# Kernel tuning notes

Measured on AMD Instinct MI355X. Metric: run time of the kernel, lower is better.

Reference implementation:

```python
import jax, jax.numpy as jnp
import numpy as np

EMBED_SIZE = 768
HEAD_SIZE = 64
B, T = 4, 2048


def setup_inputs() -> dict:
    key = jax.random.key(0)
    kx, kk, kq, kv = jax.random.split(key, 4)
    x = jax.random.normal(kx, (B, T, EMBED_SIZE), dtype=jnp.float32)
    # torch Linear(E, H, bias=False): weight [H, E]; stored here as [E, H] for x @ W
    s = 1.0 / np.sqrt(EMBED_SIZE)
    Wk = jax.random.uniform(kk, (EMBED_SIZE, HEAD_SIZE), jnp.float32, -s, s)
    Wq = jax.random.uniform(kq, (EMBED_SIZE, HEAD_SIZE), jnp.float32, -s, s)
    Wv = jax.random.uniform(kv, (EMBED_SIZE, HEAD_SIZE), jnp.float32, -s, s)
    return {"x": x, "Wk": Wk, "Wq": Wq, "Wv": Wv}


def reference(x, Wk, Wq, Wv):
    Bx, Tx, E = x.shape
    k = x @ Wk  # [B, T, H]
    q = x @ Wq
    v = x @ Wv
    w = jnp.einsum("bth,bsh->bts", q, k)  # [B, T, T]
    causal = jnp.tril(jnp.ones((Tx, Tx), dtype=bool))
    # Faithful to source: mask to -inf FIRST, then scale by sqrt(embed_size)
    w = jnp.where(causal, w, -jnp.inf)
    w = w / jnp.sqrt(jnp.asarray(E, dtype=x.dtype))
    w = jax.nn.softmax(w, axis=-1)
    # dropout: eval mode / identity for the correctness baseline
    return jnp.einsum("bts,bsh->bth", w, v)
```

## Files before the change

kernel.cpp:

```cpp
#include <hip/hip_runtime.h>
#include <hip/hip_bf16.h>


typedef __attribute__((ext_vector_type(8))) short short8;
typedef __attribute__((ext_vector_type(4))) float f32x4;

#define SPLIT_KB 8
#define MAX_SP 5

__device__ __forceinline__ unsigned short f2bf(float f) {
    union { float f; unsigned u; } v; v.f = f;
    unsigned r = v.u + 0x7fffu + ((v.u >> 16) & 1u);
    return (unsigned short)(r >> 16);
}

__global__ __launch_bounds__(256) void wt_kernel(const float* __restrict__ Wk,
                                                 const float* __restrict__ Wq,
                                                 const float* __restrict__ Wv,
                                                 unsigned short* __restrict__ WT) {
    const float CSCALE = 1.4426950408889634f / 27.712812921102035f;
    int flat = blockIdx.x * 256 + threadIdx.x;
    int k = flat / 192, n = flat % 192;
    int mat = n >> 6, col = n & 63;
    const float* W = (mat == 0) ? Wq : (mat == 1) ? Wk : Wv;
    float v = W[k * 64 + col];
    if (mat == 0) v *= CSCALE;
    WT[n * 768 + k] = f2bf(v);
}

__global__ __launch_bounds__(256) void proj_kernel(const float* __restrict__ x,
                                                   const unsigned short* __restrict__ WT,
                                                   unsigned short* __restrict__ qws,
                                                   unsigned short* __restrict__ kws,
                                                   unsigned short* __restrict__ vT) {
    __shared__ unsigned short xs[64 * 72];
    __shared__ unsigned short wsm[64 * 72];
    int tid = threadIdx.x;
    int lane = tid & 63, wave = tid >> 6;
    int quad = lane >> 4, l16 = lane & 15;
    int wm = wave & 1, wn = wave >> 1;
    int row0 = blockIdx.x * 64;
    int my = blockIdx.y;

    f32x4 acc[2][2];
    for (int mt = 0; mt < 2; ++mt)
        for (int nt = 0; nt < 2; ++nt) acc[mt][nt] = (f32x4)(0.f);

    for (int kc = 0; kc < 12; ++kc) {
        __syncthreads();
        for (int i = 0; i < 2; ++i) {
            int e = tid + 256 * i;
            int row = e >> 3, hb = (e & 7) * 8;
            const float* src = x + (size_t)(row0 + row) * 768 + kc * 64 + hb;
            float4 f0 = *(const float4*)(src);
            float4 f1 = *(const float4*)(src + 4);
            short8 pk;
            pk[0] = (short)f2bf(f0.x); pk[1] = (short)f2bf(f0.y);
            pk[2] = (short)f2bf(f0.z); pk[3] = (short)f2bf(f0.w);
            pk[4] = (short)f2bf(f1.x); pk[5] = (short)f2bf(f1.y);
            pk[6] = (short)f2bf(f1.z); pk[7] = (short)f2bf(f1.w);
            *(short8*)&xs[row * 72 + hb] = pk;
        }
        for (int i = 0; i < 2; ++i) {
            int e = tid + 256 * i;
            int n = e >> 3, kb8 = (e & 7) * 8;
            *(short8*)&wsm[n * 72 + kb8] =
                *(const short8*)&WT[(size_t)(my * 64 + n) * 768 + kc * 64 + kb8];
        }
        __syncthreads();
        for (int kh = 0; kh < 2; ++kh) {
            int kk = kh * 32 + quad * 8;
            short8 a[2], bfr[2];
            for (int mt = 0; mt < 2; ++mt)
                a[mt] = *(const short8*)&xs[(wm * 32 + mt * 16 + l16) * 72 + kk];
            for (int nt = 0; nt < 2; ++nt)
                bfr[nt] = *(const short8*)&wsm[(wn * 32 + nt * 16 + l16) * 72 + kk];
            for (int mt = 0; mt < 2; ++mt)
                for (int nt = 0; nt < 2; ++nt)
                    acc[mt][nt] = __builtin_amdgcn_mfma_f32_16x16x32_bf16(
                        a[mt], bfr[nt], acc[mt][nt], 0, 0, 0);
        }
    }
    __syncthreads();
    for (int mt = 0; mt < 2; ++mt) {
        for (int nt = 0; nt < 2; ++nt) {
            int n = wn * 32 + nt * 16 + l16;
            for (int j = 0; j < 4; ++j) {
                int rloc = wm * 32 + mt * 16 + quad * 4 + j;
                unsigned short bv = f2bf(acc[mt][nt][j]);
                if (my == 0)      qws[(size_t)(row0 + rloc) * 64 + n] = bv;
                else if (my == 1) kws[(size_t)(row0 + rloc) * 64 + n] = bv;
                else              xs[n * 72 + rloc] = bv;
            }
        }
    }
    if (my == 2) {
        __syncthreads();
        int bidx = row0 >> 11, t0 = row0 & 2047;
        for (int i = 0; i < 2; ++i) {
            int e = tid + 256 * i;
            int c = e >> 3, rb = (e & 7) * 8;
            *(short8*)&vT[((size_t)(bidx * 64 + c)) * 2048 + t0 + rb] =
                *(const short8*)&xs[c * 72 + rb];
        }
    }
}

__global__ __launch_bounds__(128) void attn_split(const unsigned short* __restrict__ qws,
                                                  const unsigned short* __restrict__ kws,
                                                  const unsigned short* __restrict__ vT,
                                                  float* __restrict__ po,
                                                  float* __restrict__ pm,
                                                  float* __restrict__ pl) {
    int bx = blockIdx.x, b = blockIdx.y, sp = blockIdx.z;
    int kbmax = (bx >> 1) + 1;
    int nsp = (kbmax + SPLIT_KB - 1) / SPLIT_KB;
    if (sp >= nsp) return;
    int kb_lo = sp * SPLIT_KB;
    int kb_hi = min(kb_lo + SPLIT_KB, kbmax);

    __shared__ unsigned short qs[32 * 72];
    __shared__ unsigned short ks[64 * 72];
    __shared__ unsigned short vs[64 * 72];
    __shared__ unsigned short ps[2][16 * 72];
    int tid = threadIdx.x;
    int lane = tid & 63, wave = tid >> 6;
    int quad = lane >> 4, l16 = lane & 15;
    int q0 = bx * 32;
    size_t qbase = ((size_t)b * 2048 + q0) * 64;
    for (int i = 0; i < 2; ++i) {
        int e = tid + 128 * i;
        int r = e >> 3, hb = (e & 7) * 8;
        *(short8*)&qs[r * 72 + hb] = *(const short8*)&qws[qbase + r * 64 + hb];
    }
    __syncthreads();
    short8 aq[2];
    for (int kh = 0; kh < 2; ++kh)
        aq[kh] = *(const short8*)&qs[(wave * 16 + l16) * 72 + kh * 32 + quad * 8];

    f32x4 o_acc[4];
    for (int nt = 0; nt < 4; ++nt) o_acc[nt] = (f32x4)(0.f);
    float m_run[4], l_run[4];
    int row_g[4];
    for (int j = 0; j < 4; ++j) {
        m_run[j] = -1e30f; l_run[j] = 0.f;
        row_g[j] = q0 + wave * 16 + quad * 4 + j;
    }

    for (int kb = kb_lo; kb < kb_hi; ++kb) {
        __syncthreads();
        size_t kvbase = ((size_t)b * 2048 + kb * 64) * 64;
        for (int i = 0; i < 4; ++i) {
            int e = tid + 128 * i;
            int r = e >> 3, hb = (e & 7) * 8;
            *(short8*)&ks[r * 72 + hb] = *(const short8*)&kws[kvbase + r * 64 + hb];
        }
        for (int i = 0; i < 4; ++i) {
            int e = tid + 128 * i;
            int h = e >> 3, kyb = (e & 7) * 8;
            *(short8*)&vs[h * 72 + kyb] =
                *(const short8*)&vT[((size_t)b * 64 + h) * 2048 + kb * 64 + kyb];
        }
        __syncthreads();
        f32x4 s[4];
        for (int nt = 0; nt < 4; ++nt) s[nt] = (f32x4)(0.f);
        for (int kh = 0; kh < 2; ++kh)
            for (int nt = 0; nt < 4; ++nt) {
                short8 bk = *(const short8*)&ks[(nt * 16 + l16) * 72 + kh * 32 + quad * 8];
                s[nt] = __builtin_amdgcn_mfma_f32_16x16x32_bf16(aq[kh], bk, s[nt], 0, 0, 0);
            }
        if (kb == kbmax - 1) {
            for (int nt = 0; nt < 4; ++nt) {
                int key = kb * 64 + nt * 16 + l16;
                for (int j = 0; j < 4; ++j)
                    if (key > row_g[j]) s[nt][j] = -1e30f;
            }
        }
        float mx[4], al[4], rs[4];
        for (int j = 0; j < 4; ++j)
            mx[j] = fmaxf(fmaxf(s[0][j], s[1][j]), fmaxf(s[2][j], s[3][j]));
        for (int off = 1; off < 16; off <<= 1)
            for (int j = 0; j < 4; ++j)
                mx[j] = fmaxf(mx[j], __shfl_xor(mx[j], off, 16));
        for (int j = 0; j < 4; ++j) {
            float mn = fmaxf(m_run[j], mx[j]);
            al[j] = exp2f(m_run[j] - mn);
            m_run[j] = mn;
            rs[j] = 0.f;
        }
        for (int nt = 0; nt < 4; ++nt)
            for (int j = 0; j < 4; ++j) {
                float p = exp2f(s[nt][j] - m_run[j]);
                rs[j] += p;
                ps[wave][(quad * 4 + j) * 72 + nt * 16 + l16] = f2bf(p);
            }
        for (int off = 1; off < 16; off <<= 1)
            for (int j = 0; j < 4; ++j)
                rs[j] += __shfl_xor(rs[j], off, 16);
        for (int j = 0; j < 4; ++j) l_run[j] = l_run[j] * al[j] + rs[j];
        for (int nt = 0; nt < 4; ++nt)
            for (int j = 0; j < 4; ++j) o_acc[nt][j] *= al[j];
        for (int kh = 0; kh < 2; ++kh) {
            short8 ap = *(const short8*)&ps[wave][l16 * 72 + kh * 32 + quad * 8];
            for (int nt = 0; nt < 4; ++nt) {
                short8 bv = *(const short8*)&vs[(nt * 16 + l16) * 72 + kh * 32 + quad * 8];
                o_acc[nt] = __builtin_amdgcn_mfma_f32_16x16x32_bf16(ap, bv, o_acc[nt], 0, 0, 0);
            }
        }
    }
    int sbase = ((b * 64 + bx) * MAX_SP + sp) * 32;
    for (int nt = 0; nt < 4; ++nt)
        for (int j = 0; j < 4; ++j) {
            int r = wave * 16 + quad * 4 + j;
            po[(size_t)(sbase + r) * 64 + nt * 16 + l16] = o_acc[nt][j];
        }
    if (l16 == 0) {
        for (int j = 0; j < 4; ++j) {
            int r = wave * 16 + quad * 4 + j;
            pm[sbase + r] = m_run[j];
            pl[sbase + r] = l_run[j];
        }
    }
}

__global__ __launch_bounds__(256) void reduce_kernel(const float* __restrict__ po,
                                                     const float* __restrict__ pm,
                                                     const float* __restrict__ pl,
                                                     float* __restrict__ out) {
    int tid = threadIdx.x;
    int lane = tid & 63, wave = tid >> 6;
    int g = blockIdx.x * 4 + wave;
    int b = g >> 11, t = g & 2047;
    int bx = t >> 5, r = t & 31;
    int kbmax = (bx >> 1) + 1;
    int nsp = (kbmax + SPLIT_KB - 1) / SPLIT_KB;
    int base = ((b * 64 + bx) * MAX_SP) * 32 + r;
    float mstar = -1e30f;
    for (int sp = 0; sp < nsp; ++sp)
        mstar = fmaxf(mstar, pm[base + sp * 32]);
    float acc = 0.f, lsum = 0.f;
    for (int sp = 0; sp < nsp; ++sp) {
        float w = exp2f(pm[base + sp * 32] - mstar);
        acc += w * po[(size_t)(base + sp * 32) * 64 + lane];
        lsum += w * pl[base + sp * 32];
    }
    out[(size_t)g * 64 + lane] = acc / lsum;
}

extern "C" void kernel_launch(void* const* d_in, const int* in_sizes, int n_in,
                              void* d_out, int out_size, void* d_ws, size_t ws_size,
                              hipStream_t stream) {
    const float* x  = (const float*)d_in[0];
    const float* Wk = (const float*)d_in[1];
    const float* Wq = (const float*)d_in[2];
    const float* Wv = (const float*)d_in[3];
    float* out = (float*)d_out;
    char* w = (char*)d_ws;
    unsigned short* WT  = (unsigned short*)w;
    unsigned short* qws = (unsigned short*)(w + 294912);
    unsigned short* kws = (unsigned short*)(w + 1343488);
    unsigned short* vT  = (unsigned short*)(w + 2392064);
    float* po = (float*)(w + 3440640);
    float* pm = (float*)(w + 13926400);
    float* pl = (float*)(w + 14090240);
    wt_kernel<<<576, 256, 0, stream>>>(Wk, Wq, Wv, WT);
    proj_kernel<<<dim3(128, 3), 256, 0, stream>>>(x, WT, qws, kws, vT);
    attn_split<<<dim3(64, 4, MAX_SP), 128, 0, stream>>>(qws, kws, vT, po, pm, pl);
    reduce_kernel<<<2048, 256, 0, stream>>>(po, pm, pl, out);
}
```

Baseline: 119.5 us.

## Fuse weight conversion into projection, finer KV split, bypass reduce for single-split rows

Removes the separate weight transpose/convert kernel and has the projection kernel load and convert fp32 weights to bf16 directly, using 32-row tiles so twice as many blocks launch. Halves the attention split size and raises the maximum split count to spread causal work over more blocks. Query tiles needing only one split now write normalized output directly and the reduce kernel skips them. Each projection block redundantly reconverts weights, and the finer split adds more partial-output traffic for long rows.

Result: faster. 109.8 us (-8.2%).

```diff
diff --git a/kernel.cpp b/kernel.cpp
--- a/kernel.cpp
+++ b/kernel.cpp
@@ -5,8 +5,8 @@
 typedef __attribute__((ext_vector_type(8))) short short8;
 typedef __attribute__((ext_vector_type(4))) float f32x4;
 
-#define SPLIT_KB 8
-#define MAX_SP 5
+#define SPLIT_KB 4
+#define MAX_SP 8
 
 __device__ __forceinline__ unsigned short f2bf(float f) {
     union { float f; unsigned u; } v; v.f = f;
@@ -14,44 +14,33 @@
     return (unsigned short)(r >> 16);
 }
 
-__global__ __launch_bounds__(256) void wt_kernel(const float* __restrict__ Wk,
-                                                 const float* __restrict__ Wq,
-                                                 const float* __restrict__ Wv,
-                                                 unsigned short* __restrict__ WT) {
-    const float CSCALE = 1.4426950408889634f / 27.712812921102035f;
-    int flat = blockIdx.x * 256 + threadIdx.x;
-    int k = flat / 192, n = flat % 192;
-    int mat = n >> 6, col = n & 63;
-    const float* W = (mat == 0) ? Wq : (mat == 1) ? Wk : Wv;
-    float v = W[k * 64 + col];
-    if (mat == 0) v *= CSCALE;
-    WT[n * 768 + k] = f2bf(v);
-}
-
 __global__ __launch_bounds__(256) void proj_kernel(const float* __restrict__ x,
-                                                   const unsigned short* __restrict__ WT,
+                                                   const float* __restrict__ Wk,
+                                                   const float* __restrict__ Wq,
+                                                   const float* __restrict__ Wv,
                                                    unsigned short* __restrict__ qws,
                                                    unsigned short* __restrict__ kws,
                                                    unsigned short* __restrict__ vT) {
-    __shared__ unsigned short xs[64 * 72];
+    __shared__ unsigned short xs[32 * 72];
     __shared__ unsigned short wsm[64 * 72];
+    const float CSCALE = 1.4426950408889634f / 27.712812921102035f;
     int tid = threadIdx.x;
     int lane = tid & 63, wave = tid >> 6;
     int quad = lane >> 4, l16 = lane & 15;
-    int wm = wave & 1, wn = wave >> 1;
-    int row0 = blockIdx.x * 64;
+    int row0 = blockIdx.x * 32;
     int my = blockIdx.y;
-
-    f32x4 acc[2][2];
-    for (int mt = 0; mt < 2; ++mt)
-        for (int nt = 0; nt < 2; ++nt) acc[mt][nt] = (f32x4)(0.f);
+    const float* W = (my == 0) ? Wq : (my == 1) ? Wk : Wv;
+
+    int xrow = tid >> 3, xcb = (tid & 7) * 8;
+    int wn = tid & 63, wk0 = (tid >> 6) * 16;
+
+    f32x4 acc[2];
+    acc[0] = (f32x4)(0.f); acc[1] = (f32x4)(0.f);
 
     for (int kc = 0; kc < 12; ++kc) {
         __syncthreads();
-        for (int i = 0; i < 2; ++i) {
-            int e = tid + 256 * i;
-            int row = e >> 3, hb = (e & 7) * 8;
-            const float* src = x + (size_t)(row0 + row) * 768 + kc * 64 + hb;
+        {
+            const float* src = x + (size_t)(row0 + xrow) * 768 + kc * 64 + xcb;
             float4 f0 = *(const float4*)(src);
             float4 f1 = *(const float4*)(src + 4);
             short8 pk;
@@ -59,50 +48,49 @@
             pk[2] = (short)f2bf(f0.z); pk[3] = (short)f2bf(f0.w);
             pk[4] = (short)f2bf(f1.x); pk[5] = (short)f2bf(f1.y);
             pk[6] = (short)f2bf(f1.z); pk[7] = (short)f2bf(f1.w);
-            *(short8*)&xs[row * 72 + hb] = pk;
-        }
-        for (int i = 0; i < 2; ++i) {
-            int e = tid + 256 * i;
-            int n = e >> 3, kb8 = (e & 7) * 8;
-            *(short8*)&wsm[n * 72 + kb8] =
-                *(const short8*)&WT[(size_t)(my * 64 + n) * 768 + kc * 64 + kb8];
+            *(short8*)&xs[xrow * 72 + xcb] = pk;
+        }
+        {
+            float wv[16];
+            for (int i = 0; i < 16; ++i)
+                wv[i] = W[(size_t)(kc * 64 + wk0 + i) * 64 + wn];
+            if (my == 0)
+                for (int i = 0; i < 16; ++i) wv[i] *= CSCALE;
+            short8 p0, p1;
+            for (int i = 0; i < 8; ++i) { p0[i] = (short)f2bf(wv[i]); p1[i] = (short)f2bf(wv[8 + i]); }
+            *(short8*)&wsm[wn * 72 + wk0] = p0;
+            *(short8*)&wsm[wn * 72 + wk0 + 8] = p1;
         }
         __syncthreads();
         for (int kh = 0; kh < 2; ++kh) {
             int kk = kh * 32 + quad * 8;
-            short8 a[2], bfr[2];
-            for (int mt = 0; mt < 2; ++mt)
-                a[mt] = *(const short8*)&xs[(wm * 32 + mt * 16 + l16) * 72 + kk];
-            for (int nt = 0; nt < 2; ++nt)
-                bfr[nt] = *(const short8*)&wsm[(wn * 32 + nt * 16 + l16) * 72 + kk];
-            for (int mt = 0; mt < 2; ++mt)
-                for (int nt = 0; nt < 2; ++nt)
-                    acc[mt][nt] = __builtin_amdgcn_mfma_f32_16x16x32_bf16(
-                        a[mt], bfr[nt], acc[mt][nt], 0, 0, 0);
+            short8 bfr = *(const short8*)&wsm[(wave * 16 + l16) * 72 + kk];
+            for (int mt = 0; mt < 2; ++mt) {
+                short8 a = *(const short8*)&xs[(mt * 16 + l16) * 72 + kk];
+                acc[mt] = __builtin_amdgcn_mfma_f32_16x16x32_bf16(a, bfr, acc[mt], 0, 0, 0);
+            }
         }
     }
     __syncthreads();
-    for (int mt = 0; mt < 2; ++mt) {
-        for (int nt = 0; nt < 2; ++nt) {
-            int n = wn * 32 + nt * 16 + l16;
+    int n = wave * 16 + l16;
+    if (my != 2) {
+        unsigned short* dst = (my == 0) ? qws : kws;
+        for (int mt = 0; mt < 2; ++mt)
             for (int j = 0; j < 4; ++j) {
-                int rloc = wm * 32 + mt * 16 + quad * 4 + j;
-                unsigned short bv = f2bf(acc[mt][nt][j]);
-                if (my == 0)      qws[(size_t)(row0 + rloc) * 64 + n] = bv;
-                else if (my == 1) kws[(size_t)(row0 + rloc) * 64 + n] = bv;
-                else              xs[n * 72 + rloc] = bv;
-            }
-        }
-    }
-    if (my == 2) {
+                int rloc = mt * 16 + quad * 4 + j;
+                dst[(size_t)(row0 + rloc) * 64 + n] = f2bf(acc[mt][j]);
+            }
+    } else {
+        for (int mt = 0; mt < 2; ++mt)
+            for (int j = 0; j < 4; ++j) {
+                int rloc = mt * 16 + quad * 4 + j;
+                wsm[n * 40 + rloc] = f2bf(acc[mt][j]);
+            }
         __syncthreads();
         int bidx = row0 >> 11, t0 = row0 & 2047;
-        for (int i = 0; i < 2; ++i) {
-            int e = tid + 256 * i;
-            int c = e >> 3, rb = (e & 7) * 8;
-            *(short8*)&vT[((size_t)(bidx * 64 + c)) * 2048 + t0 + rb] =
-                *(const short8*)&xs[c * 72 + rb];
-        }
+        int c = tid >> 2, rb = (tid & 3) * 8;
+        *(short8*)&vT[((size_t)(bidx * 64 + c)) * 2048 + t0 + rb] =
+            *(const short8*)&wsm[c * 40 + rb];
     }
 }
 
@@ -111,7 +99,8 @@
                                                   const unsigned short* __restrict__ vT,
                                                   float* __restrict__ po,
                                                   float* __restrict__ pm,
-                                                  float* __restrict__ pl) {
+                                                  float* __restrict__ pl,
+                                                  float* __restrict__ out) {
     int bx = blockIdx.x, b = blockIdx.y, sp = blockIdx.z;
     int kbmax = (bx >> 1) + 1;
     int nsp = (kbmax + SPLIT_KB - 1) / SPLIT_KB;
@@ -208,6 +197,13 @@
             }
         }
     }
+    if (nsp == 1) {
+        for (int nt = 0; nt < 4; ++nt)
+            for (int j = 0; j < 4; ++j)
+                out[((size_t)b * 2048 + row_g[j]) * 64 + nt * 16 + l16] =
+                    o_acc[nt][j] / l_run[j];
+        return;
+    }
     int sbase = ((b * 64 + bx) * MAX_SP + sp) * 32;
     for (int nt = 0; nt < 4; ++nt)
         for (int j = 0; j < 4; ++j) {
@@ -234,6 +230,7 @@
     int bx = t >> 5, r = t & 31;
     int kbmax = (bx >> 1) + 1;
     int nsp = (kbmax + SPLIT_KB - 1) / SPLIT_KB;
+    if (nsp == 1) return;
     int base = ((b * 64 + bx) * MAX_SP) * 32 + r;
     float mstar = -1e30f;
     for (int sp = 0; sp < nsp; ++sp)
@@ -256,15 +253,13 @@
     const float* Wv = (const float*)d_in[3];
     float* out = (float*)d_out;
     char* w = (char*)d_ws;
-    unsigned short* WT  = (unsigned short*)w;
-    unsigned short* qws = (unsigned short*)(w + 294912);
-    unsigned short* kws = (unsigned short*)(w + 1343488);
-    unsigned short* vT  = (unsigned short*)(w + 2392064);
-    float* po = (float*)(w + 3440640);
-    float* pm = (float*)(w + 13926400);
-    float* pl = (float*)(w + 14090240);
-    wt_kernel<<<576, 256, 0, stream>>>(Wk, Wq, Wv, WT);
-    proj_kernel<<<dim3(128, 3), 256, 0, stream>>>(x, WT, qws, kws, vT);
-    attn_split<<<dim3(64, 4, MAX_SP), 128, 0, stream>>>(qws, kws, vT, po, pm, pl);
+    unsigned short* qws = (unsigned short*)w;
+    unsigned short* kws = (unsigned short*)(w + 1048576);
+    unsigned short* vT  = (unsigned short*)(w + 2097152);
+    float* po = (float*)(w + 3145728);
+    float* pm = (float*)(w + 19922944);
+    float* pl = (float*)(w + 20185088);
+    proj_kernel<<<dim3(256, 3), 256, 0, stream>>>(x, Wk, Wq, Wv, qws, kws, vT);
+    attn_split<<<dim3(64, 4, MAX_SP), 128, 0, stream>>>(qws, kws, vT, po, pm, pl, out);
     reduce_kernel<<<2048, 256, 0, stream>>>(po, pm, pl, out);
 }
```
